# Optimization experiments

Measured on AMD Instinct MI355X. Metric: run time of the kernel, lower is better.

Reference implementation:

```python
import jax, jax.numpy as jnp
import numpy as np

B, S, HIDDEN, N_HEADS = 1, 2048, 2048, 16
HEAD_DIM = HIDDEN // N_HEADS  # 128


def setup_inputs() -> dict:
    key = jax.random.key(0)
    ks = jax.random.split(key, 7)
    w = 0.02  # init scale for projection weights
    return {
        "x_self": jax.random.normal(ks[0], (B, S, HIDDEN), jnp.float32),
        "x_cross": jax.random.normal(ks[1], (B, S, HIDDEN), jnp.float32),
        "mask": jnp.zeros((B, 1, S, S), jnp.float32),
        "Wq": jax.random.normal(ks[2], (HIDDEN, HIDDEN), jnp.float32) * w,
        "Wk": jax.random.normal(ks[3], (HIDDEN, HIDDEN), jnp.float32) * w,
        "Wv": jax.random.normal(ks[4], (HIDDEN, HIDDEN), jnp.float32) * w,
        "Wo": jax.random.normal(ks[5], (HIDDEN, HIDDEN), jnp.float32) * w,
    }


def reference(x_self, x_cross, mask, Wq, Wk, Wv, Wo):
    bf16 = jnp.bfloat16
    b = x_self.shape[0]
    scale = HEAD_DIM ** -0.5

    def split_heads(x):  # [b, s, hidden] -> [b, h, s, d]
        return x.reshape(b, -1, N_HEADS, HEAD_DIM).transpose(0, 2, 1, 3)

    # projections run in bf16 (weights cast to bf16 in the original)
    q_self = split_heads((x_self.astype(bf16) @ Wq.astype(bf16).T))
    q_cross = split_heads((x_cross.astype(bf16) @ Wq.astype(bf16).T))
    # k/v for both self and cross blocks come from x_self with identical weights
    k = split_heads((x_self.astype(bf16) @ Wk.astype(bf16).T))
    v = split_heads((x_self.astype(bf16) @ Wv.astype(bf16).T))

    def attn_block(qh):
        # fp32 upcast for QK^T + softmax, then bf16 cast for AV (dropout p=0 -> identity)
        w = jnp.einsum('bhqd,bhkd->bhqk', qh.astype(jnp.float32), k.astype(jnp.float32)) * scale
        w = w + mask
        w = jax.nn.softmax(w, axis=-1).astype(bf16)
        return jnp.einsum('bhqk,bhkd->bhqd', w, v.astype(bf16))  # [b, h, s, d] bf16

    out_self = attn_block(q_self)
    out_cross = attn_block(q_cross)
    out = jnp.concatenate([out_self, out_cross], axis=1)          # [b, 2h, s, d]
    out_flat = out.transpose(0, 2, 1, 3).reshape(b, -1, HIDDEN)   # [b, 2s, hidden]
    Wo_bf = Wo.astype(bf16)
    out_final = 0.5 * (out_flat @ Wo_bf.T + out_flat @ Wo_bf.T)
    return out_final.astype(jnp.float32)
```

## Files before the change

### kernel.cpp

```cpp
#include <hip/hip_runtime.h>
#include <hip/hip_bf16.h>
#include <stdint.h>

#define S 2048
#define HID 2048
#define NH 16
#define HD 128

typedef short short8 __attribute__((ext_vector_type(8)));
typedef float f32x4 __attribute__((ext_vector_type(4)));
typedef float f32x16 __attribute__((ext_vector_type(16)));
typedef uint32_t u32;
typedef u32 u32x4 __attribute__((ext_vector_type(4)));

__device__ __forceinline__ ushort f2bf(float x) {
  uint32_t u = __builtin_bit_cast(uint32_t, x);
  if ((u & 0x7fffffffu) > 0x7f800000u) return (ushort)((u >> 16) | 0x40);
  uint32_t r = u + 0x7fffu + ((u >> 16) & 1u);
  return (ushort)(r >> 16);
}
__device__ __forceinline__ float bf2f(ushort u) {
  union { uint32_t i; float f; } c; c.i = ((uint32_t)u) << 16; return c.f;
}

__device__ __forceinline__ void glds16(const ushort* g, ushort* l) {
  __builtin_amdgcn_global_load_lds((const __attribute__((address_space(1))) uint32_t*)g,
                                   (__attribute__((address_space(3))) uint32_t*)l, 16, 0, 0);
}

__device__ __forceinline__ void mfma16(f32x4& d, short8 a, short8 b) {
  asm volatile("v_mfma_f32_16x16x32_bf16 %0, %1, %2, %0" : "+v"(d) : "v"(a), "v"(b));
}
__device__ __forceinline__ void mfma32(f32x16& d, short8 a, short8 b) {
  asm volatile("v_mfma_f32_32x32x16_bf16 %0, %1, %2, %0" : "+v"(d) : "v"(a), "v"(b));
}
#define MFMA_FENCE() do {                              \
    asm volatile("s_nop 7\n\ts_nop 7\n\ts_nop 7");     \
    __builtin_amdgcn_sched_barrier(0);                 \
  } while (0)
__device__ __forceinline__ void plswap(u32& a, u32& b) {
  asm volatile("v_permlane32_swap_b32 %0, %1" : "+v"(a), "+v"(b));
}
__device__ __forceinline__ u32 cvtpk(float lo, float hi) {
  u32 r; asm volatile("v_cvt_pk_bf16_f32 %0, %1, %2" : "=v"(r) : "v"(lo), "v"(hi)); return r;
}

struct CastArgs { const float* s[6]; ushort* d[6]; };
__global__ __launch_bounds__(256) void cast6_k(CastArgs a) {
  const float* in = a.s[blockIdx.y];
  ushort* out = a.d[blockIdx.y];
  int i = blockIdx.x * 256 + threadIdx.x;
  float4 v = ((const float4*)in)[i];
  ushort4 o;
  o.x = f2bf(v.x); o.y = f2bf(v.y); o.z = f2bf(v.z); o.w = f2bf(v.w);
  ((ushort4*)out)[i] = o;
}

template <int OUTF32, int NSPLIT>
__global__ __launch_bounds__(256)
void gemm_bt_k(const ushort* __restrict__ A, const ushort* __restrict__ B,
               void* __restrict__ C, int M, int N, int K) {
  __shared__ __align__(16) ushort ldsA[128 * 64];
  __shared__ __align__(16) ushort ldsB[128 * 64];
  const int tid = threadIdx.x, lane = tid & 63, wid = tid >> 6;
  const int g = lane >> 4, c = lane & 15;
  const int wr = wid >> 1, wc = wid & 1;
  const long m0 = (long)blockIdx.y * 128, n0 = (long)blockIdx.x * 128;
  const int srow = lane >> 3, sslot = lane & 7;

  f32x4 acc[4][4] = {};

  for (int k0 = 0; k0 < K; k0 += 64) {
#pragma unroll
    for (int i = 0; i < 4; ++i) {
      int ii = wid * 4 + i;
      int rt = ii * 8 + srow;
      int col = ((sslot ^ (rt & 7)) << 3) + k0;
      glds16(A + (m0 + rt) * (long)K + col, ldsA + ii * 512);
      glds16(B + (n0 + rt) * (long)K + col, ldsB + ii * 512);
    }
    __syncthreads();
#pragma unroll
    for (int kk = 0; kk < 2; ++kk) {
      short8 af[4], bfr[4];
#pragma unroll
      for (int m = 0; m < 4; ++m) {
        int row = wr * 64 + m * 16 + c;
        af[m] = *(const short8*)(ldsA + row * 64 + (((kk * 4 + g) ^ (row & 7)) << 3));
      }
#pragma unroll
      for (int n = 0; n < 4; ++n) {
        int row = wc * 64 + n * 16 + c;
        bfr[n] = *(const short8*)(ldsB + row * 64 + (((kk * 4 + g) ^ (row & 7)) << 3));
      }
#pragma unroll
      for (int m = 0; m < 4; ++m)
#pragma unroll
        for (int n = 0; n < 4; ++n) mfma16(acc[m][n], af[m], bfr[n]);
    }
    __syncthreads();
  }
  MFMA_FENCE();
#pragma unroll
  for (int m = 0; m < 4; ++m) {
#pragma unroll
    for (int r = 0; r < 4; ++r) {
      long grow = m0 + wr * 64 + m * 16 + g * 4 + r;
#pragma unroll
      for (int n = 0; n < 4; ++n) {
        long gcol = n0 + wc * 64 + n * 16 + c;
        long idx;
        if (NSPLIT) idx = ((gcol >> 11) << 22) + (grow << 11) + (gcol & 2047);
        else        idx = grow * N + gcol;
        float v = acc[m][n][r];
        if (OUTF32) ((float*)C)[idx] = bf2f(f2bf(v));
        else        ((ushort*)C)[idx] = f2bf(v);
      }
    }
  }
}

__global__ __launch_bounds__(256)
void transpose_bf16_k(const ushort* __restrict__ in, ushort* __restrict__ out) {
  __shared__ __align__(16) ushort t[64][72];
  const int tid = threadIdx.x;
  const long bx = (long)blockIdx.x * 64;
  const long by = (long)blockIdx.y * 64;
#pragma unroll
  for (int i = 0; i < 2; ++i) {
    int row = (tid >> 3) + i * 32;
    int col = (tid & 7) * 8;
    *(short8*)(&t[row][col]) = *(const short8*)(in + (by + row) * 2048 + bx + col);
  }
  __syncthreads();
#pragma unroll
  for (int i = 0; i < 2; ++i) {
    int orow = (tid >> 3) + i * 32;
    int ocol = (tid & 7) * 8;
    short8 v;
#pragma unroll
    for (int j = 0; j < 8; ++j) v[j] = (short)t[ocol + j][orow];
    *(short8*)(out + (bx + orow) * 2048 + by + ocol) = v;
  }
}

__global__ __launch_bounds__(256)
void attn4_k(const ushort* __restrict__ Qself, const ushort* __restrict__ Qcross,
             const ushort* __restrict__ Kp, const ushort* __restrict__ Vt,
             const float* __restrict__ mask, ushort* __restrict__ outf) {
  __shared__ __align__(16) ushort ldsK[2 * 64 * 128];
  __shared__ __align__(16) ushort ldsV[2 * 128 * 64];
  const int tid = threadIdx.x, lane = tid & 63, wid = tid >> 6;
  const int c31 = lane & 31, hi = lane >> 5;

  const int b = blockIdx.x;
  const int xcd = b & 7, j = b >> 3;
  const int h = xcd + 8 * (j & 1);
  const int blk = (j >> 1) & 1;
  const int qt = j >> 2;

  const ushort* Qp = blk ? Qcross : Qself;
  const int qbase = qt * 128 + wid * 32;
  const long qme = qbase + c31;

  short8 qf[8];
#pragma unroll
  for (int ks = 0; ks < 8; ++ks)
    qf[ks] = *(const short8*)(Qp + qme * HID + h * HD + ks * 16 + hi * 8);

  f32x16 o[4] = {};
  float m_r = -__builtin_inff(), l_r = 0.f;

  const float SC  = 0.08838834764831845f;
  const float L2E = 1.4426950408889634f;
  const float THR = 5.545177444479562f;

  const int kRow4 = lane >> 4, kSlot = lane & 15;
  const int vRow8 = lane >> 3, vSlot = lane & 7;
  const float* mrow = mask + qme * (long)S;

#define STAGE(BO, KV0) do {                                                       \
    _Pragma("unroll")                                                             \
    for (int i_ = 0; i_ < 4; ++i_) {                                              \
      int seg = i_ * 4 + wid;                                                     \
      int rk = seg * 4 + kRow4;                                                   \
      glds16(Kp + (long)((KV0) + rk) * HID + h * HD + ((kSlot ^ (rk & 15)) << 3), \
             ldsK + (BO) * 8192 + seg * 512);                                     \
      int rv = seg * 8 + vRow8;                                                   \
      glds16(Vt + (long)(h * HD + rv) * S + (KV0) + ((vSlot ^ (rv & 7)) << 3),    \
             ldsV + (BO) * 8192 + seg * 512);                                     \
    }                                                                             \
  } while (0)

  STAGE(0, 0);
  __syncthreads();

  for (int t = 0; t < 32; ++t) {
    const int bo = t & 1;
    const ushort* kb = ldsK + bo * 8192;
    const ushort* vb = ldsV + bo * 8192;
    if (t < 31) STAGE(bo ^ 1, (t + 1) * 64);
    const int kv0 = t * 64;

    f32x4 mv[2][4];
#pragma unroll
    for (int kvb = 0; kvb < 2; ++kvb)
#pragma unroll
      for (int rg = 0; rg < 4; ++rg)
        mv[kvb][rg] = *(const f32x4*)(mrow + kv0 + kvb * 32 + rg * 8 + hi * 4);

    f32x16 s0 = {}, s1 = {};
    __builtin_amdgcn_s_setprio(1);
#pragma unroll
    for (int ks = 0; ks < 8; ++ks) {
      int r0 = c31, r1 = 32 + c31;
      short8 kf0 = *(const short8*)(kb + r0 * 128 + (((ks * 2 + hi) ^ (r0 & 15)) << 3));
      short8 kf1 = *(const short8*)(kb + r1 * 128 + (((ks * 2 + hi) ^ (r1 & 15)) << 3));
      mfma32(s0, kf0, qf[ks]);
      mfma32(s1, kf1, qf[ks]);
    }
    __builtin_amdgcn_s_setprio(0);
    MFMA_FENCE();

#pragma unroll
    for (int r = 0; r < 16; ++r) {
      s0[r] = __builtin_fmaf(s0[r], SC, mv[0][r >> 2][r & 3]);
      s1[r] = __builtin_fmaf(s1[r], SC, mv[1][r >> 2][r & 3]);
    }

    float mx[16];
#pragma unroll
    for (int r = 0; r < 16; ++r) mx[r] = fmaxf(s0[r], s1[r]);
#pragma unroll
    for (int st = 8; st >= 1; st >>= 1)
#pragma unroll
      for (int i = 0; i < 8; ++i)
        if (i < st) mx[i] = fmaxf(mx[i], mx[i + st]);
    float pmax = fmaxf(mx[0], __shfl_xor(mx[0], 32));

    if (!__all(pmax <= m_r + THR)) {
      float mnew = fmaxf(m_r, pmax);
      float alpha = __builtin_amdgcn_exp2f((m_r - mnew) * L2E);
      m_r = mnew;
      l_r *= alpha;
#pragma unroll
      for (int r = 0; r < 16; ++r) {
        float alf = __shfl(alpha, (r & 3) + 8 * (r >> 2) + 4 * hi);
#pragma unroll
        for (int dt = 0; dt < 4; ++dt) o[dt][r] *= alf;
      }
    }

    const float nm = -m_r * L2E;
#pragma unroll
    for (int r = 0; r < 16; ++r) {
      s0[r] = __builtin_amdgcn_exp2f(__builtin_fmaf(s0[r], L2E, nm));
      s1[r] = __builtin_amdgcn_exp2f(__builtin_fmaf(s1[r], L2E, nm));
    }
    float sm[16];
#pragma unroll
    for (int r = 0; r < 16; ++r) sm[r] = s0[r] + s1[r];
#pragma unroll
    for (int st = 8; st >= 1; st >>= 1)
#pragma unroll
      for (int i = 0; i < 8; ++i)
        if (i < st) sm[i] += sm[i + st];
    l_r += sm[0] + __shfl_xor(sm[0], 32);

    short8 pa[4];
#pragma unroll
    for (int kk = 0; kk < 4; ++kk) {
      const f32x16& sv = (kk < 2) ? s0 : s1;
      const int bq = (kk & 1) * 8;
      u32 x0 = cvtpk(sv[bq + 0], sv[bq + 1]);
      u32 x1 = cvtpk(sv[bq + 2], sv[bq + 3]);
      u32 y0 = cvtpk(sv[bq + 4], sv[bq + 5]);
      u32 y1 = cvtpk(sv[bq + 6], sv[bq + 7]);
      plswap(x0, y0);
      plswap(x1, y1);
      u32x4 tt; tt[0] = x0; tt[1] = x1; tt[2] = y0; tt[3] = y1;
      pa[kk] = __builtin_bit_cast(short8, tt);
    }
    asm volatile("s_nop 1");
    __builtin_amdgcn_sched_barrier(0);

    __builtin_amdgcn_s_setprio(1);
#pragma unroll
    for (int dt = 0; dt < 4; ++dt) {
      int row = dt * 32 + c31;
#pragma unroll
      for (int kk = 0; kk < 4; ++kk) {
        short8 vf = *(const short8*)(vb + row * 64 + (((kk * 2 + hi) ^ (row & 7)) << 3));
        mfma32(o[dt], pa[kk], vf);
      }
    }
    __builtin_amdgcn_s_setprio(0);

    __syncthreads();
  }
#undef STAGE

  MFMA_FENCE();
#pragma unroll
  for (int r = 0; r < 16; ++r) {
    int qr = (r & 3) + 8 * (r >> 2) + 4 * hi;
    float linv = 1.0f / __shfl(l_r, qr);
    long orow = 2L * (qbase + qr) + blk;
#pragma unroll
    for (int dt = 0; dt < 4; ++dt)
      outf[orow * HID + h * HD + dt * 32 + c31] = f2bf(o[dt][r] * linv);
  }
}

extern "C" void kernel_launch(void* const* d_in, const int* in_sizes, int n_in,
                              void* d_out, int out_size, void* d_ws, size_t ws_size,
                              hipStream_t stream) {
  (void)in_sizes; (void)n_in; (void)out_size; (void)ws_size;
  const float* x_self  = (const float*)d_in[0];
  const float* x_cross = (const float*)d_in[1];
  const float* mask    = (const float*)d_in[2];
  const float* Wq      = (const float*)d_in[3];
  const float* Wk      = (const float*)d_in[4];
  const float* Wv      = (const float*)d_in[5];
  const float* Wo      = (const float*)d_in[6];

  uint8_t* w = (uint8_t*)d_ws;
  const size_t MB8 = (size_t)S * HID * sizeof(ushort);
  ushort* xs_bf   = (ushort*)(w + 0 * MB8);
  ushort* xc_bf   = (ushort*)(w + 1 * MB8);
  ushort* Wq_bf   = (ushort*)(w + 2 * MB8);
  ushort* Wk_bf   = (ushort*)(w + 3 * MB8);
  ushort* Wv_bf   = (ushort*)(w + 4 * MB8);
  ushort* Wo_bf   = (ushort*)(w + 5 * MB8);
  ushort* q_self  = (ushort*)(w + 6 * MB8);
  ushort* q_cross = (ushort*)(w + 7 * MB8);
  ushort* k_      = (ushort*)(w + 8 * MB8);
  ushort* v_      = (ushort*)(w + 9 * MB8);
  ushort* vt       = xs_bf;
  ushort* out_flat = Wq_bf;

  CastArgs ca;
  ca.s[0] = x_self;  ca.d[0] = xs_bf;
  ca.s[1] = x_cross; ca.d[1] = xc_bf;
  ca.s[2] = Wq;      ca.d[2] = Wq_bf;
  ca.s[3] = Wk;      ca.d[3] = Wk_bf;
  ca.s[4] = Wv;      ca.d[4] = Wv_bf;
  ca.s[5] = Wo;      ca.d[5] = Wo_bf;
  cast6_k<<<dim3(4096, 6), 256, 0, stream>>>(ca);

  gemm_bt_k<0, 0><<<dim3(16, 32), 256, 0, stream>>>(xs_bf, Wq_bf, q_self, 4096, 2048, 2048);
  gemm_bt_k<0, 1><<<dim3(32, 16), 256, 0, stream>>>(xs_bf, Wk_bf, k_, 2048, 4096, 2048);

  transpose_bf16_k<<<dim3(32, 32), 256, 0, stream>>>(v_, vt);

  attn4_k<<<dim3(512), 256, 0, stream>>>(q_self, q_cross, k_, vt, mask, out_flat);

  gemm_bt_k<1, 0><<<dim3(16, 32), 256, 0, stream>>>(out_flat, Wo_bf, d_out, 4096, 2048, 2048);
}
```

Before: 256.7 us.

## Pre-transpose attention mask to bf16 for coalesced per-tile loads

Adds a kernel that converts the fp32 mask to bf16 and transposes it to key-major layout. The attention kernel then reads mask values where adjacent lanes (adjacent query rows) hit adjacent addresses, instead of each lane streaming its own fp32 row. This halves the bytes per mask read and is meant to cut the mask traffic that every head and q-tile repeats. In exchange it adds an extra launch and more scalar loads per tile, and rounding the mask to bf16 loses precision for general non-zero masks.

```diff
diff --git a/kernel.cpp b/kernel.cpp
--- a/kernel.cpp
+++ b/kernel.cpp
@@ -145,9 +145,34 @@
 }
 
 __global__ __launch_bounds__(256)
+void maskT_k(const float* __restrict__ in, ushort* __restrict__ out) {
+  __shared__ ushort t[64][72];
+  const int tid = threadIdx.x;
+  const long q0 = (long)blockIdx.y * 64;
+  const long k0 = (long)blockIdx.x * 64;
+#pragma unroll
+  for (int i = 0; i < 4; ++i) {
+    int row = i * 16 + (tid >> 4);
+    int col = (tid & 15) * 4;
+    float4 v = *(const float4*)(in + (q0 + row) * S + k0 + col);
+    t[col + 0][row] = f2bf(v.x);
+    t[col + 1][row] = f2bf(v.y);
+    t[col + 2][row] = f2bf(v.z);
+    t[col + 3][row] = f2bf(v.w);
+  }
+  __syncthreads();
+#pragma unroll
+  for (int i = 0; i < 2; ++i) {
+    int row = i * 32 + (tid >> 3);
+    int col = (tid & 7) * 8;
+    *(short8*)(out + (k0 + row) * S + q0 + col) = *(const short8*)(&t[row][col]);
+  }
+}
+
+__global__ __launch_bounds__(256)
 void attn4_k(const ushort* __restrict__ Qself, const ushort* __restrict__ Qcross,
              const ushort* __restrict__ Kp, const ushort* __restrict__ Vt,
-             const float* __restrict__ mask, ushort* __restrict__ outf) {
+             const ushort* __restrict__ maskT, ushort* __restrict__ outf) {
   __shared__ __align__(16) ushort ldsK[2 * 64 * 128];
   __shared__ __align__(16) ushort ldsV[2 * 128 * 64];
   const int tid = threadIdx.x, lane = tid & 63, wid = tid >> 6;
@@ -177,7 +202,7 @@
 
   const int kRow4 = lane >> 4, kSlot = lane & 15;
   const int vRow8 = lane >> 3, vSlot = lane & 7;
-  const float* mrow = mask + qme * (long)S;
+  const ushort* mT = maskT + qme;
 
 #define STAGE(BO, KV0) do {                                                       \
     _Pragma("unroll")                                                             \
@@ -202,12 +227,13 @@
     if (t < 31) STAGE(bo ^ 1, (t + 1) * 64);
     const int kv0 = t * 64;
 
-    f32x4 mv[2][4];
-#pragma unroll
-    for (int kvb = 0; kvb < 2; ++kvb)
-#pragma unroll
-      for (int rg = 0; rg < 4; ++rg)
-        mv[kvb][rg] = *(const f32x4*)(mrow + kv0 + kvb * 32 + rg * 8 + hi * 4);
+    ushort mvu0[16], mvu1[16];
+#pragma unroll
+    for (int r = 0; r < 16; ++r) {
+      int krow = (r & 3) + 8 * (r >> 2) + 4 * hi;
+      mvu0[r] = mT[(long)(kv0 + krow) * S];
+      mvu1[r] = mT[(long)(kv0 + 32 + krow) * S];
+    }
 
     f32x16 s0 = {}, s1 = {};
     __builtin_amdgcn_s_setprio(1);
@@ -224,8 +250,8 @@
 
 #pragma unroll
     for (int r = 0; r < 16; ++r) {
-      s0[r] = __builtin_fmaf(s0[r], SC, mv[0][r >> 2][r & 3]);
-      s1[r] = __builtin_fmaf(s1[r], SC, mv[1][r >> 2][r & 3]);
+      s0[r] = __builtin_fmaf(s0[r], SC, bf2f(mvu0[r]));
+      s1[r] = __builtin_fmaf(s1[r], SC, bf2f(mvu1[r]));
     }
 
     float mx[16];
@@ -338,6 +364,7 @@
   ushort* v_      = (ushort*)(w + 9 * MB8);
   ushort* vt       = xs_bf;
   ushort* out_flat = Wq_bf;
+  ushort* maskT    = v_;
 
   CastArgs ca;
   ca.s[0] = x_self;  ca.d[0] = xs_bf;
@@ -352,8 +379,9 @@
   gemm_bt_k<0, 1><<<dim3(32, 16), 256, 0, stream>>>(xs_bf, Wk_bf, k_, 2048, 4096, 2048);
 
   transpose_bf16_k<<<dim3(32, 32), 256, 0, stream>>>(v_, vt);
-
-  attn4_k<<<dim3(512), 256, 0, stream>>>(q_self, q_cross, k_, vt, mask, out_flat);
+  maskT_k<<<dim3(32, 32), 256, 0, stream>>>(mask, maskT);
+
+  attn4_k<<<dim3(512), 256, 0, stream>>>(q_self, q_cross, k_, vt, maskT, out_flat);
 
   gemm_bt_k<1, 0><<<dim3(16, 32), 256, 0, stream>>>(out_flat, Wo_bf, d_out, 4096, 2048, 2048);
 }
```

Result: no change. 253.4 us (-1.3%).
